# Kernel optimization log

Measured on AMD Instinct MI355X. Metric: run time of the kernel, lower is better.

The kernel has to match this reference:

```python
import jax, jax.numpy as jnp
import numpy as np

LAMBDA_W = 1.0
NEG_INF = -1e10


def setup_inputs() -> dict:
    key = jax.random.key(0)
    k1, k2, k3 = jax.random.split(key, 3)
    B, L, D = 8, 2048, 256
    h_x = jax.random.normal(k1, (B, L, D), dtype=jnp.float32)
    h_y = jax.random.normal(k2, (B, L, D), dtype=jnp.float32)
    # masks: valid prefix of 3/4 length, padded tail of zeros (exercises masking)
    valid = (3 * L) // 4
    base = (jnp.arange(L) < valid).astype(jnp.float32)
    x_mask = jnp.broadcast_to(base, (B, L))
    y_mask = jnp.broadcast_to(base, (B, L))
    # biaffine weight (n_label=1, no biases), init_value scaling kept at O(1)
    W = jax.random.normal(k3, (D, D), dtype=jnp.float32) / jnp.sqrt(jnp.float32(D))
    return {"h_x": h_x, "h_y": h_y, "x_mask": x_mask, "y_mask": y_mask, "W": W}


def reference(h_x, h_y, x_mask, y_mask, W):
    # src = h_x [B,Ls,D], pred = h_y [B,Lp,D]
    src, pred = h_x, h_y
    src_mask, pred_mask = x_mask, y_mask

    # cost_mx[b,p,s] = ||src[b,s] - pred[b,p]||_2, via ||a||^2+||b||^2-2ab
    src_sq = jnp.sum(src * src, axis=-1)            # [B,Ls]
    pred_sq = jnp.sum(pred * pred, axis=-1)         # [B,Lp]
    cross = jnp.einsum('bpd,bsd->bps', pred, src)   # [B,Lp,Ls]
    cost_mx = jnp.sqrt(jnp.maximum(pred_sq[:, :, None] + src_sq[:, None, :] - 2.0 * cross, 0.0))

    # biaffine scores: pred W src^T  -> [B,Lp,Ls]
    tr_mx = jnp.einsum('bpd,de,bse->bps', pred, W, src)

    # cost_mask[b,p,s] = pred_mask[b,p]*src_mask[b,s]
    cost_mask = pred_mask[:, :, None] * src_mask[:, None, :]
    tr_mx = jnp.where(cost_mask == 0, NEG_INF, tr_mx)
    tr_prob = jax.nn.softmax(tr_mx, axis=-1)

    flow_cost = tr_prob * cost_mx                   # [B,Lp,Ls]

    nL1 = jnp.sum(pred_mask, axis=-1, keepdims=True)  # [B,1]
    nL2 = jnp.sum(src_mask, axis=-1, keepdims=True)   # [B,1]
    fc = jnp.sum(flow_cost, axis=(1, 2), keepdims=True)  # [B,1,1]
    fc = fc / (nL1 * nL2)   # broadcasts [B,1,1]/[B,1] -> [B,B,1], matches torch
    fc = jnp.mean(fc)
    return fc * LAMBDA_W
```

## Files before the change

kernel.cpp:

```cpp
#include <hip/hip_runtime.h>
#include <math.h>
#include <stdint.h>

#define B_ 8
#define L_ 2048
#define D_ 256
#define NEG_INF_V (-1e10f)
#define NSTRIP 16
#define PITCH 140

typedef __bf16 bf16x8 __attribute__((ext_vector_type(8)));
typedef __bf16 bf16x4 __attribute__((ext_vector_type(4)));
typedef float f32x4 __attribute__((ext_vector_type(4)));

#define MFMA16(a, b, c) __builtin_amdgcn_mfma_f32_16x16x32_bf16((a), (b), (c), 0, 0, 0)


__global__ __launch_bounds__(256) void convert_kernel(
    const float* __restrict__ x, const float* __restrict__ y,
    const float* __restrict__ W,
    __bf16* __restrict__ srcFM, __bf16* __restrict__ predFM,
    __bf16* __restrict__ WFM,
    float* __restrict__ src_sq, float* __restrict__ pred_sq) {
    int tid = threadIdx.x;
    int blk = blockIdx.x;
    if (blk < 2048) {
        const float* in = (blk < 1024) ? x : y;
        __bf16* out = (blk < 1024) ? srcFM : predFM;
        float* sqout = (blk < 1024) ? src_sq : pred_sq;
        int g = blk & 1023;
        __shared__ __align__(16) __bf16 sFM[512 * 8];
        __shared__ float sSQ[16];
        int kb = (tid & 31) >> 2, qq = tid & 3;
        #pragma unroll
        for (int pass = 0; pass < 2; ++pass) {
            int m = pass * 8 + (tid >> 5);
            const float* p = in + ((size_t)g * 16 + m) * D_ + (tid & 31) * 8;
            float4 v0 = *(const float4*)p;
            float4 v1 = *(const float4*)(p + 4);
            float ss = v0.x * v0.x + v0.y * v0.y + v0.z * v0.z + v0.w * v0.w +
                       v1.x * v1.x + v1.y * v1.y + v1.z * v1.z + v1.w * v1.w;
            #pragma unroll
            for (int o = 16; o > 0; o >>= 1) ss += __shfl_xor(ss, o, 64);
            if ((tid & 31) == 0) sSQ[m] = ss;
            union { __bf16 o[8]; bf16x8 v; } cv;
            cv.o[0] = (__bf16)v0.x; cv.o[1] = (__bf16)v0.y;
            cv.o[2] = (__bf16)v0.z; cv.o[3] = (__bf16)v0.w;
            cv.o[4] = (__bf16)v1.x; cv.o[5] = (__bf16)v1.y;
            cv.o[6] = (__bf16)v1.z; cv.o[7] = (__bf16)v1.w;
            *(bf16x8*)(sFM + (m * 32 + kb * 4 + qq) * 8) = cv.v;
        }
        __syncthreads();
        int G0 = tid * 2;
        int kb0 = G0 >> 6, q0 = (G0 >> 4) & 3, m0 = G0 & 15;
        bf16x8 a = *(const bf16x8*)(sFM + (m0 * 32 + kb0 * 4 + q0) * 8);
        bf16x8 bgr = *(const bf16x8*)(sFM + ((m0 + 1) * 32 + kb0 * 4 + q0) * 8);
        *(bf16x8*)(out + ((size_t)g * 512 + G0) * 8) = a;
        *(bf16x8*)(out + ((size_t)g * 512 + G0 + 1) * 8) = bgr;
        if (tid < 16) sqout[g * 16 + tid] = sSQ[tid];
    } else {
        int idx = (blk - 2048) * 256 + tid;
        int m = idx & 15, q = (idx >> 4) & 3, kb = (idx >> 6) & 7, gn = idx >> 9;
        union { __bf16 o[8]; bf16x8 v; } cv;
        #pragma unroll
        for (int j = 0; j < 8; ++j)
            cv.o[j] = (__bf16)W[(size_t)(kb * 32 + q * 8 + j) * D_ + gn * 16 + m];
        *(bf16x8*)(WFM + (size_t)idx * 8) = cv.v;
    }
}

__global__ __launch_bounds__(256, 2) void predw_mfma(
    const __bf16* __restrict__ predFM, const __bf16* __restrict__ WFM,
    const float* __restrict__ pred_mask, __bf16* __restrict__ pwFM) {
    __shared__ __align__(16) __bf16 sT[128 * 136];
    __shared__ int flag;
    int tid = threadIdx.x, lane = tid & 63, wid = tid >> 6;
    int wp = wid >> 1, wn = wid & 1;
    int id = blockIdx.x;
    int m0 = (((id >> 3) & 15) + (id & 7) * 16) * 128;
    int n0 = (id >> 7) * 128;
    if (tid == 0) flag = 0;
    __syncthreads();
    if (tid < 128) { if (pred_mask[m0 + tid] != 0.f) atomicOr(&flag, 1); }
    __syncthreads();
    if (!flag) return;

    const __bf16* bA = predFM + (size_t)(m0 / 16 + wp * 4) * 4096 + lane * 8;
    const __bf16* bB = WFM + (size_t)(n0 / 16 + wn * 4) * 4096 + lane * 8;
    f32x4 acc[4][4] = {};
    #pragma unroll
    for (int kb = 0; kb < 8; ++kb) {
        bf16x8 fA[4], fB[4];
        #pragma unroll
        for (int t = 0; t < 4; ++t) {
            fA[t] = *(const bf16x8*)(bA + (t * 8 + kb) * 512);
            fB[t] = *(const bf16x8*)(bB + (t * 8 + kb) * 512);
        }
        #pragma unroll
        for (int pt = 0; pt < 4; ++pt)
            #pragma unroll
            for (int st = 0; st < 4; ++st)
                acc[pt][st] = MFMA16(fA[pt], fB[st], acc[pt][st]);
    }
    int q = lane >> 4, cn = lane & 15;
    #pragma unroll
    for (int pt = 0; pt < 4; ++pt)
        #pragma unroll
        for (int st = 0; st < 4; ++st)
            #pragma unroll
            for (int r = 0; r < 4; ++r)
                sT[(wp * 64 + pt * 16 + q * 4 + r) * 136 + wn * 64 + st * 16 + cn] =
                    (__bf16)acc[pt][st][r];
    __syncthreads();
    #pragma unroll
    for (int i = 0; i < 8; ++i) {
        int idx = i * 256 + tid;
        int gl = idx >> 8, kbl = (idx >> 6) & 3, qq = (idx >> 4) & 3, mm = idx & 15;
        bf16x8 v = *(const bf16x8*)(sT + (gl * 16 + mm) * 136 + kbl * 32 + qq * 8);
        *(bf16x8*)(pwFM +
                   (((size_t)(m0 / 16 + gl) * 8 + n0 / 32 + kbl) * 64 + qq * 16 + mm) * 8) = v;
    }
}

__global__ __launch_bounds__(256, 3) void fused_mfma(
    const __bf16* __restrict__ srcFM, const __bf16* __restrict__ predFM,
    const __bf16* __restrict__ pwFM,
    const float* __restrict__ src_mask, const float* __restrict__ pred_mask,
    const float* __restrict__ src_sq, const float* __restrict__ pred_sq,
    float* __restrict__ m_part, float* __restrict__ l_part,
    float* __restrict__ w_part, float* __restrict__ Sarr,
    unsigned int* __restrict__ counter) {
    __shared__ __align__(16) __bf16 sT[64 * PITCH];
    __shared__ __align__(16) __bf16 sGm[64 * PITCH];
    __shared__ float sPM[64], sPSQ[64], sSM[128], sSSQ[128];
    __shared__ int flg[4];
    int tid = threadIdx.x, lane = tid & 63, wid = tid >> 6;
    int role = wid >> 1, ws = wid & 1;
    int id = blockIdx.x;
    int b = id & 7, px = (id >> 3) & 31, sy = id >> 8;
    int p0 = px * 64;

    if (id == 0) {
        if (tid == 0) *counter = 0u;
        if (tid < 24) Sarr[tid] = 0.f;
    }
    if (tid < 4) flg[tid] = 0;
    __syncthreads();
    if (tid < 64) {
        float v = pred_mask[b * L_ + p0 + tid];
        sPM[tid] = v;
        sPSQ[tid] = pred_sq[b * L_ + p0 + tid];
        atomicOr(&flg[(v != 0.f) ? 0 : 1], 1);
    } else if (tid < 192) {
        int t = tid - 64;
        float v = src_mask[b * L_ + sy * 128 + t];
        sSM[t] = v;
        sSSQ[t] = src_sq[b * L_ + sy * 128 + t];
        atomicOr(&flg[(v != 0.f) ? 2 : 3], 1);
    }
    __syncthreads();
    const bool anyVP = flg[0] != 0, anyIP = flg[1] != 0;
    const bool anyVS = flg[2] != 0, allVS = flg[3] == 0;
    const bool doT = anyVP && anyVS;
    const bool doG = anyVS || anyIP;
    if (!doT && !doG) {
        if (tid < 64) {
            size_t o = ((size_t)(b * L_ + p0 + tid)) * NSTRIP + sy;
            m_part[o] = NEG_INF_V; l_part[o] = 0.f; w_part[o] = 0.f;
        }
        return;
    }

    int q = lane >> 4, cn = lane & 15;
    const __bf16* bB = srcFM + ((size_t)(b * 128 + sy * 8 + ws * 4)) * 4096 + lane * 8;
    const __bf16* bA = (role == 0 ? pwFM : predFM) +
                       ((size_t)(b * 128 + px * 4)) * 4096 + lane * 8;
    f32x4 acc[4][4] = {};
    if (role == 1 || doT) {
        #pragma unroll
        for (int kb = 0; kb < 8; ++kb) {
            bf16x8 fA[4], fB[4];
            #pragma unroll
            for (int t = 0; t < 4; ++t) {
                fA[t] = *(const bf16x8*)(bA + (t * 8 + kb) * 512);
                fB[t] = *(const bf16x8*)(bB + (t * 8 + kb) * 512);
            }
            #pragma unroll
            for (int pt = 0; pt < 4; ++pt)
                #pragma unroll
                for (int st = 0; st < 4; ++st)
                    acc[pt][st] = MFMA16(fA[pt], fB[st], acc[pt][st]);
        }
        __bf16* dst = (role == 0 ? sT : sGm) + (size_t)q * 4 * PITCH + ws * 64 + cn;
        #pragma unroll
        for (int pt = 0; pt < 4; ++pt)
            #pragma unroll
            for (int st = 0; st < 4; ++st)
                #pragma unroll
                for (int r = 0; r < 4; ++r)
                    dst[(pt * 16 + r) * PITCH + st * 16] = (__bf16)acc[pt][st][r];
    }
    __syncthreads();

    int half = lane >> 5, l5 = lane & 31, c0 = l5 * 4;
    float smv[4], sqv[4];
    #pragma unroll
    for (int j = 0; j < 4; ++j) {
        smv[j] = sSM[c0 + j];
        sqv[j] = sSSQ[c0 + j];
    }
    #pragma unroll
    for (int i = 0; i < 8; ++i) {
        int row = wid * 16 + i * 2 + half;
        float pm = sPM[row], psq = sPSQ[row];
        float rM, rL, rW;
        if (pm != 0.f && !doT) {
            rM = NEG_INF_V; rL = 0.f; rW = 0.f;
        } else {
            bf16x4 gv4 = *(const bf16x4*)(sGm + (size_t)row * PITCH + c0);
            float cst[4];
            #pragma unroll
            for (int j = 0; j < 4; ++j) {
                float cc = psq + sqv[j] - 2.f * (float)gv4[j];
                cst[j] = sqrtf(fmaxf(cc, 0.f));
            }
            if (pm != 0.f) {
                bf16x4 tv4 = *(const bf16x4*)(sT + (size_t)row * PITCH + c0);
                float tv[4];
                #pragma unroll
                for (int j = 0; j < 4; ++j) {
                    float t = (float)tv4[j];
                    tv[j] = (allVS || smv[j] != 0.f) ? t : NEG_INF_V;
                }
                float tm = fmaxf(fmaxf(tv[0], tv[1]), fmaxf(tv[2], tv[3]));
                #pragma unroll
                for (int o = 16; o > 0; o >>= 1) tm = fmaxf(tm, __shfl_xor(tm, o, 32));
                float l = 0.f, w = 0.f;
                #pragma unroll
                for (int j = 0; j < 4; ++j) {
                    float e = __expf(tv[j] - tm);
                    l += e;
                    w = fmaf(e, cst[j], w);
                }
                #pragma unroll
                for (int o = 16; o > 0; o >>= 1) {
                    l += __shfl_xor(l, o, 32);
                    w += __shfl_xor(w, o, 32);
                }
                rM = tm; rL = l; rW = w;
            } else {
                float w = cst[0] + cst[1] + cst[2] + cst[3];
                #pragma unroll
                for (int o = 16; o > 0; o >>= 1) w += __shfl_xor(w, o, 32);
                rM = NEG_INF_V; rL = 128.f; rW = w;
            }
        }
        if (l5 == 0) {
            size_t o = ((size_t)(b * L_ + p0 + row)) * NSTRIP + sy;
            m_part[o] = rM; l_part[o] = rL; w_part[o] = rW;
        }
    }
}

__global__ __launch_bounds__(256) void combine_kernel(
    const float* __restrict__ m_part, const float* __restrict__ l_part,
    const float* __restrict__ w_part,
    const float* __restrict__ x_mask, const float* __restrict__ y_mask,
    float* __restrict__ Sarr, unsigned int* __restrict__ counter,
    float* __restrict__ out) {
    int tid = threadIdx.x;
    int r = blockIdx.x * 256 + tid;
    int b = r >> 11;
    size_t base = (size_t)r * NSTRIP;
    float mm = -1e30f;
    #pragma unroll
    for (int s = 0; s < NSTRIP; ++s) mm = fmaxf(mm, m_part[base + s]);
    float l = 0.f, w = 0.f;
    #pragma unroll
    for (int s = 0; s < NSTRIP; ++s) {
        float e = __expf(m_part[base + s] - mm);
        l = fmaf(l_part[base + s], e, l);
        w = fmaf(w_part[base + s], e, w);
    }
    float sv = w / l;
    float n1 = y_mask[r], n2 = x_mask[r];
    __shared__ float red[3][256];
    red[0][tid] = sv; red[1][tid] = n1; red[2][tid] = n2;
    __syncthreads();
    for (int o = 128; o > 0; o >>= 1) {
        if (tid < o) {
            red[0][tid] += red[0][tid + o];
            red[1][tid] += red[1][tid + o];
            red[2][tid] += red[2][tid + o];
        }
        __syncthreads();
    }
    __shared__ int isLast;
    if (tid == 0) {
        atomicAdd(&Sarr[b], red[0][0]);
        atomicAdd(&Sarr[8 + b], red[1][0]);
        atomicAdd(&Sarr[16 + b], red[2][0]);
        __threadfence();
        isLast = (atomicAdd(counter, 1u) == 63u) ? 1 : 0;
    }
    __syncthreads();
    if (isLast) {
        __shared__ float fb[24];
        if (tid < 24) fb[tid] = atomicAdd(&Sarr[tid], 0.f);
        __syncthreads();
        if (tid == 0) {
            float ss = 0.f, si = 0.f;
            for (int bb = 0; bb < B_; bb++) {
                ss += fb[bb];
                si += 1.0f / (fb[8 + bb] * fb[16 + bb]);
            }
            out[0] = ss * si / (float)(B_ * B_);
        }
    }
}

extern "C" void kernel_launch(void* const* d_in, const int* in_sizes, int n_in,
                              void* d_out, int out_size, void* d_ws, size_t ws_size,
                              hipStream_t stream) {
    const float* h_x = (const float*)d_in[0];
    const float* h_y = (const float*)d_in[1];
    const float* x_mask = (const float*)d_in[2];
    const float* y_mask = (const float*)d_in[3];
    const float* W = (const float*)d_in[4];

    char* w8 = (char*)d_ws;
    const size_t BLD2 = (size_t)B_ * L_ * D_ * 2;
    __bf16* srcFM = (__bf16*)w8;
    __bf16* predFM = (__bf16*)(w8 + BLD2);
    __bf16* pwFM = (__bf16*)(w8 + 2 * BLD2);
    __bf16* WFM = (__bf16*)(w8 + 3 * BLD2);
    float* src_sq = (float*)(w8 + 3 * BLD2 + (1 << 17));
    float* pred_sq = (float*)(w8 + 3 * BLD2 + (1 << 17) + (1 << 16));
    char* pbase = w8 + 3 * BLD2 + (1 << 17) + (1 << 17);
    const size_t PSZ = (size_t)B_ * L_ * NSTRIP * 4;
    float* m_part = (float*)pbase;
    float* l_part = (float*)(pbase + PSZ);
    float* w_part = (float*)(pbase + 2 * PSZ);
    float* Sarr = (float*)(pbase + 3 * PSZ);
    unsigned int* counter = (unsigned int*)(pbase + 3 * PSZ + 128);

    convert_kernel<<<2080, 256, 0, stream>>>(h_x, h_y, W, srcFM, predFM, WFM,
                                             src_sq, pred_sq);
    predw_mfma<<<256, 256, 0, stream>>>(predFM, WFM, y_mask, pwFM);
    fused_mfma<<<4096, 256, 0, stream>>>(
        srcFM, predFM, pwFM, x_mask, y_mask, src_sq, pred_sq,
        m_part, l_part, w_part, Sarr, counter);
    combine_kernel<<<B_ * L_ / 256, 256, 0, stream>>>(
        m_part, l_part, w_part, x_mask, y_mask, Sarr, counter, (float*)d_out);
}
```

Baseline: 160.0 us.

## Compute both GEMMs per wave and reduce softmax directly from MFMA registers

Each wave now owns a 16-row slab of pred rows and computes both the distance cross-product and biaffine-score tiles against all 128 source columns. The softmax/flow reduction then runs straight from the MFMA accumulators using 16-lane shuffles. This removes the shared-memory staging of bf16 tiles, the block barrier and the extra bf16 rounding of the scores. In exchange it needs more accumulator registers and reloads the source fragments in every wave, and the masked-row handling is reworked, which changes the partial values written for fully masked tiles.

```diff
diff --git a/kernel.cpp b/kernel.cpp
--- a/kernel.cpp
+++ b/kernel.cpp
@@ -7,10 +7,8 @@
 #define D_ 256
 #define NEG_INF_V (-1e10f)
 #define NSTRIP 16
-#define PITCH 140
 
 typedef __bf16 bf16x8 __attribute__((ext_vector_type(8)));
-typedef __bf16 bf16x4 __attribute__((ext_vector_type(4)));
 typedef float f32x4 __attribute__((ext_vector_type(4)));
 
 #define MFMA16(a, b, c) __builtin_amdgcn_mfma_f32_16x16x32_bf16((a), (b), (c), 0, 0, 0)
@@ -130,12 +128,9 @@
     float* __restrict__ m_part, float* __restrict__ l_part,
     float* __restrict__ w_part, float* __restrict__ Sarr,
     unsigned int* __restrict__ counter) {
-    __shared__ __align__(16) __bf16 sT[64 * PITCH];
-    __shared__ __align__(16) __bf16 sGm[64 * PITCH];
     __shared__ float sPM[64], sPSQ[64], sSM[128], sSSQ[128];
     __shared__ int flg[4];
     int tid = threadIdx.x, lane = tid & 63, wid = tid >> 6;
-    int role = wid >> 1, ws = wid & 1;
     int id = blockIdx.x;
     int b = id & 7, px = (id >> 3) & 31, sy = id >> 8;
     int p0 = px * 64;
@@ -159,105 +154,92 @@
         atomicOr(&flg[(v != 0.f) ? 2 : 3], 1);
     }
     __syncthreads();
-    const bool anyVP = flg[0] != 0, anyIP = flg[1] != 0;
-    const bool anyVS = flg[2] != 0, allVS = flg[3] == 0;
+    const bool anyVP = flg[0] != 0, anyIP = flg[1] != 0, anyVS = flg[2] != 0;
     const bool doT = anyVP && anyVS;
     const bool doG = anyVS || anyIP;
-    if (!doT && !doG) {
+    if (!doG) {
         if (tid < 64) {
             size_t o = ((size_t)(b * L_ + p0 + tid)) * NSTRIP + sy;
-            m_part[o] = NEG_INF_V; l_part[o] = 0.f; w_part[o] = 0.f;
+            m_part[o] = NEG_INF_V; l_part[o] = 128.f; w_part[o] = 0.f;
         }
         return;
     }
 
+    const __bf16* bS = srcFM + ((size_t)(b * 128 + sy * 8)) * 4096 + lane * 8;
+    const __bf16* bP = predFM + ((size_t)(b * 128 + px * 4 + wid)) * 4096 + lane * 8;
+    const __bf16* bW = pwFM + ((size_t)(b * 128 + px * 4 + wid)) * 4096 + lane * 8;
+
+    f32x4 aT[8] = {};
+    f32x4 aG[8] = {};
+    if (doT) {
+        #pragma unroll
+        for (int kb = 0; kb < 8; ++kb) {
+            bf16x8 fP = *(const bf16x8*)(bP + kb * 512);
+            bf16x8 fW = *(const bf16x8*)(bW + kb * 512);
+            bf16x8 fB[8];
+            #pragma unroll
+            for (int t = 0; t < 8; ++t)
+                fB[t] = *(const bf16x8*)(bS + (t * 8 + kb) * 512);
+            #pragma unroll
+            for (int t = 0; t < 8; ++t) {
+                aG[t] = MFMA16(fP, fB[t], aG[t]);
+                aT[t] = MFMA16(fW, fB[t], aT[t]);
+            }
+        }
+    } else {
+        #pragma unroll
+        for (int kb = 0; kb < 8; ++kb) {
+            bf16x8 fP = *(const bf16x8*)(bP + kb * 512);
+            bf16x8 fB[8];
+            #pragma unroll
+            for (int t = 0; t < 8; ++t)
+                fB[t] = *(const bf16x8*)(bS + (t * 8 + kb) * 512);
+            #pragma unroll
+            for (int t = 0; t < 8; ++t)
+                aG[t] = MFMA16(fP, fB[t], aG[t]);
+        }
+    }
+
     int q = lane >> 4, cn = lane & 15;
-    const __bf16* bB = srcFM + ((size_t)(b * 128 + sy * 8 + ws * 4)) * 4096 + lane * 8;
-    const __bf16* bA = (role == 0 ? pwFM : predFM) +
-                       ((size_t)(b * 128 + px * 4)) * 4096 + lane * 8;
-    f32x4 acc[4][4] = {};
-    if (role == 1 || doT) {
-        #pragma unroll
-        for (int kb = 0; kb < 8; ++kb) {
-            bf16x8 fA[4], fB[4];
-            #pragma unroll
-            for (int t = 0; t < 4; ++t) {
-                fA[t] = *(const bf16x8*)(bA + (t * 8 + kb) * 512);
-                fB[t] = *(const bf16x8*)(bB + (t * 8 + kb) * 512);
-            }
-            #pragma unroll
-            for (int pt = 0; pt < 4; ++pt)
-                #pragma unroll
-                for (int st = 0; st < 4; ++st)
-                    acc[pt][st] = MFMA16(fA[pt], fB[st], acc[pt][st]);
-        }
-        __bf16* dst = (role == 0 ? sT : sGm) + (size_t)q * 4 * PITCH + ws * 64 + cn;
-        #pragma unroll
-        for (int pt = 0; pt < 4; ++pt)
-            #pragma unroll
-            for (int st = 0; st < 4; ++st)
-                #pragma unroll
-                for (int r = 0; r < 4; ++r)
-                    dst[(pt * 16 + r) * PITCH + st * 16] = (__bf16)acc[pt][st][r];
-    }
-    __syncthreads();
-
-    int half = lane >> 5, l5 = lane & 31, c0 = l5 * 4;
-    float smv[4], sqv[4];
-    #pragma unroll
-    for (int j = 0; j < 4; ++j) {
-        smv[j] = sSM[c0 + j];
-        sqv[j] = sSSQ[c0 + j];
-    }
-    #pragma unroll
-    for (int i = 0; i < 8; ++i) {
-        int row = wid * 16 + i * 2 + half;
-        float pm = sPM[row], psq = sPSQ[row];
-        float rM, rL, rW;
-        if (pm != 0.f && !doT) {
-            rM = NEG_INF_V; rL = 0.f; rW = 0.f;
-        } else {
-            bf16x4 gv4 = *(const bf16x4*)(sGm + (size_t)row * PITCH + c0);
-            float cst[4];
-            #pragma unroll
-            for (int j = 0; j < 4; ++j) {
-                float cc = psq + sqv[j] - 2.f * (float)gv4[j];
-                cst[j] = sqrtf(fmaxf(cc, 0.f));
-            }
-            if (pm != 0.f) {
-                bf16x4 tv4 = *(const bf16x4*)(sT + (size_t)row * PITCH + c0);
-                float tv[4];
-                #pragma unroll
-                for (int j = 0; j < 4; ++j) {
-                    float t = (float)tv4[j];
-                    tv[j] = (allVS || smv[j] != 0.f) ? t : NEG_INF_V;
-                }
-                float tm = fmaxf(fmaxf(tv[0], tv[1]), fmaxf(tv[2], tv[3]));
-                #pragma unroll
-                for (int o = 16; o > 0; o >>= 1) tm = fmaxf(tm, __shfl_xor(tm, o, 32));
-                float l = 0.f, w = 0.f;
-                #pragma unroll
-                for (int j = 0; j < 4; ++j) {
-                    float e = __expf(tv[j] - tm);
-                    l += e;
-                    w = fmaf(e, cst[j], w);
-                }
-                #pragma unroll
-                for (int o = 16; o > 0; o >>= 1) {
-                    l += __shfl_xor(l, o, 32);
-                    w += __shfl_xor(w, o, 32);
-                }
-                rM = tm; rL = l; rW = w;
-            } else {
-                float w = cst[0] + cst[1] + cst[2] + cst[3];
-                #pragma unroll
-                for (int o = 16; o > 0; o >>= 1) w += __shfl_xor(w, o, 32);
-                rM = NEG_INF_V; rL = 128.f; rW = w;
-            }
-        }
-        if (l5 == 0) {
-            size_t o = ((size_t)(b * L_ + p0 + row)) * NSTRIP + sy;
-            m_part[o] = rM; l_part[o] = rL; w_part[o] = rW;
+    float smv[8], sqv[8];
+    #pragma unroll
+    for (int t = 0; t < 8; ++t) {
+        smv[t] = sSM[t * 16 + cn];
+        sqv[t] = sSSQ[t * 16 + cn];
+    }
+    int rbase = wid * 16 + q * 4;
+    #pragma unroll
+    for (int r = 0; r < 4; ++r) {
+        float pm = sPM[rbase + r], psq = sPSQ[rbase + r];
+        float tv[8], cst[8];
+        float tm = -1e30f;
+        #pragma unroll
+        for (int t = 0; t < 8; ++t) {
+            cst[t] = __builtin_amdgcn_sqrtf(
+                fmaxf(psq + sqv[t] - 2.f * aG[t][r], 0.f));
+            float tt = doT ? aT[t][r] : NEG_INF_V;
+            tv[t] = (pm == 0.f) ? 0.f : (smv[t] != 0.f ? tt : NEG_INF_V);
+            tm = fmaxf(tm, tv[t]);
+        }
+        #pragma unroll
+        for (int o = 8; o > 0; o >>= 1) tm = fmaxf(tm, __shfl_xor(tm, o, 16));
+        float l = 0.f, w = 0.f;
+        #pragma unroll
+        for (int t = 0; t < 8; ++t) {
+            float e = __expf(tv[t] - tm);
+            l += e;
+            w = fmaf(e, cst[t], w);
+        }
+        #pragma unroll
+        for (int o = 8; o > 0; o >>= 1) {
+            l += __shfl_xor(l, o, 16);
+            w += __shfl_xor(w, o, 16);
+        }
+        if (cn == 0) {
+            size_t o = ((size_t)(b * L_ + p0 + rbase + r)) * NSTRIP + sy;
+            m_part[o] = tm;
+            l_part[o] = l;
+            w_part[o] = w;
         }
     }
 }
```

Result: faster. 148.8 us (-7.0%).
